# Performance work log

Measured on AMD Instinct MI355X. Metric: run time of the kernel, lower is better.

The kernel has to match this reference:

```python
import jax, jax.numpy as jnp
import numpy as np

N_NODES = 50000


def setup_inputs() -> dict:
    key = jax.random.key(0)
    k_x, k_e, k_w1, k_w2 = jax.random.split(key, 4)
    in_c, hid, out_c = 256, 128, 64
    x = jax.random.normal(k_x, (N_NODES, in_c), dtype=jnp.float32)
    edge_index = jax.random.randint(k_e, (2, 800000), 0, N_NODES, dtype=jnp.int64)
    # Glorot-ish scaled weights (faithful to GCNConv default init scale)
    W1 = jax.random.normal(k_w1, (in_c, hid), dtype=jnp.float32) * (1.0 / np.sqrt(in_c))
    b1 = jnp.zeros((hid,), dtype=jnp.float32)
    W2 = jax.random.normal(k_w2, (hid, out_c), dtype=jnp.float32) * (1.0 / np.sqrt(hid))
    b2 = jnp.zeros((out_c,), dtype=jnp.float32)
    return {"x": x, "edge_index": edge_index, "W1": W1, "b1": b1, "W2": W2, "b2": b2}


def _gcn_norm(edge_index, n_nodes):
    # Add self loops, compute symmetric normalization D^-1/2 A D^-1/2.
    loop = jnp.arange(n_nodes, dtype=edge_index.dtype)
    src = jnp.concatenate([edge_index[0], loop])
    dst = jnp.concatenate([edge_index[1], loop])
    deg = jax.ops.segment_sum(jnp.ones_like(dst, dtype=jnp.float32), dst,
                              num_segments=n_nodes)
    dis = jnp.where(deg > 0, jax.lax.rsqrt(deg), 0.0)  # deg_inv_sqrt
    norm = dis[src] * dis[dst]  # [E + N]
    return src, dst, norm


def _gcn_conv(x, W, b, src, dst, norm, n_nodes):
    h = x @ W                                  # [N, F_out] dense transform first
    msgs = h[src] * norm[:, None]              # edge-wise gather + scale
    agg = jax.ops.segment_sum(msgs, dst, num_segments=n_nodes)  # scatter-add
    return agg + b


def reference(x, edge_index, W1, b1, W2, b2):
    n = x.shape[0]
    src, dst, norm = _gcn_norm(edge_index, n)  # cached=True: same norm both layers
    h = _gcn_conv(x, W1, b1, src, dst, norm, n)
    h = jax.nn.relu(h)
    # Dropout is identity in eval mode (deterministic reference)
    return _gcn_conv(h, W2, b2, src, dst, norm, n)
```

## Files before the change

kernel.cpp:

```cpp
#include <hip/hip_runtime.h>


#define IN_C 256
#define HID 128
#define OUTC 64
#define NBLK 256

typedef __attribute__((ext_vector_type(8))) short short8;
typedef __attribute__((ext_vector_type(4))) float f32x4;

__device__ __forceinline__ void gload_lds16(const void* src, void* dst) {
    __builtin_amdgcn_global_load_lds(
        (const __attribute__((address_space(1))) unsigned int*)src,
        (__attribute__((address_space(3))) unsigned int*)dst, 16, 0, 0);
}

__device__ __forceinline__ void bf16split(float f, ushort& h, ushort& l) {
    unsigned u = __float_as_uint(f);
    h = (ushort)(u >> 16);
    float hf = __uint_as_float(u & 0xFFFF0000u);
    unsigned v = __float_as_uint(f - hf);
    l = (ushort)((v + 0x7FFF + ((v >> 16) & 1)) >> 16);
}

__device__ __forceinline__ void cvt8(float4 f0, float4 f1, short8& hi8, short8& lo8) {
    float ff[8];
    *(float4*)&ff[0] = f0; *(float4*)&ff[4] = f1;
    unsigned* hp = (unsigned*)&hi8;
    unsigned* lp = (unsigned*)&lo8;
    #pragma unroll
    for (int i = 0; i < 4; ++i) {
        unsigned u0 = __float_as_uint(ff[2 * i]), u1 = __float_as_uint(ff[2 * i + 1]);
        unsigned hf0 = u0 & 0xFFFF0000u, hf1 = u1 & 0xFFFF0000u;
        hp[i] = (u0 >> 16) | hf1;
        float r0 = ff[2 * i]     - __uint_as_float(hf0);
        float r1 = ff[2 * i + 1] - __uint_as_float(hf1);
        lp[i] = (__float_as_uint(r0) >> 16) | (__float_as_uint(r1) & 0xFFFF0000u);
    }
}

__device__ __forceinline__ ushort f2bf(float f) {
    unsigned u = __float_as_uint(f);
    return (ushort)((u + 0x7FFF + ((u >> 16) & 1)) >> 16);
}
__device__ __forceinline__ float bf2f(ushort u) {
    return __uint_as_float((unsigned)u << 16);
}

__device__ __forceinline__ int edge_at(const void* ei, long long idx, int is32) {
    return is32 ? ((const int*)ei)[idx] : (int)((const long long*)ei)[idx];
}

__device__ __forceinline__ int detect32(const void* ei) {
    const unsigned long long* p = (const unsigned long long*)ei;
    int is32 = 0;
    for (int i = 0; i < 64; ++i)
        if (p[i] >> 32) { is32 = 1; break; }
    return is32;
}

__global__ __launch_bounds__(256) void wtrans_kernel(const float* __restrict__ W1,
                                                     const float* __restrict__ W2,
                                                     ushort* __restrict__ wf1,
                                                     ushort* __restrict__ wf2,
                                                     ushort* __restrict__ h1sent,
                                                     ushort* __restrict__ h2sent) {
    int id = blockIdx.x * 256 + threadIdx.x;
    if (id < 8192) {
        int lane = id & 63, r = id >> 6;
        int pl = r & 1, nt = (r >> 1) & 7, kidx = r >> 4;
        int n = nt * 16 + (lane & 15);
        int kb = kidx * 32 + (lane >> 4) * 8;
        ushort v[8];
        #pragma unroll
        for (int j = 0; j < 8; ++j) {
            ushort h, l; bf16split(W1[(kb + j) * HID + n], h, l);
            v[j] = pl ? l : h;
        }
        *(short8*)&wf1[(size_t)id * 8] = *(short8*)v;
    } else if (id < 10240) {
        int id2 = id - 8192;
        int lane = id2 & 63, r = id2 >> 6;
        int pl = r & 1, nt = (r >> 1) & 3, kidx = r >> 3;
        int n = nt * 16 + (lane & 15);
        int kb = kidx * 32 + (lane >> 4) * 8;
        ushort v[8];
        #pragma unroll
        for (int j = 0; j < 8; ++j) {
            ushort h, l; bf16split(W2[(kb + j) * OUTC + n], h, l);
            v[j] = pl ? l : h;
        }
        *(short8*)&wf2[(size_t)id2 * 8] = *(short8*)v;
    } else if (id < 10368) {
        h1sent[id - 10240] = 0;
    } else if (id < 10432) {
        h2sent[id - 10368] = 0;
    }
}

__global__ __launch_bounds__(256) void bin_count(const void* ei,
                                                 int* __restrict__ blkcnt, int E, int nb) {
    __shared__ int h[256];
    __shared__ int s_is32;
    int t = threadIdx.x;
    h[t] = 0;
    if (t == 0) s_is32 = detect32(ei);
    __syncthreads();
    int is32 = s_is32;
    int chunk = (E + gridDim.x - 1) / gridDim.x;
    long long s0 = (long long)blockIdx.x * chunk;
    long long s1 = s0 + chunk; if (s1 > E) s1 = E;
    for (long long e = s0 + t; e < s1; e += 256) {
        int d = edge_at(ei, (long long)E + e, is32);
        atomicAdd(&h[d >> 8], 1);
    }
    __syncthreads();
    if (t < nb) blkcnt[t * NBLK + blockIdx.x] = h[t];
}

__global__ __launch_bounds__(256) void bin_scan(int* __restrict__ blkcnt,
                                                int* __restrict__ bbase, int nb) {
    __shared__ int sh[256];
    int t = threadIdx.x;
    int tot = 0;
    if (t < nb) {
        int4* p = (int4*)&blkcnt[t * NBLK];
        int run = 0;
        for (int i = 0; i < NBLK / 4; ++i) {
            int4 v = p[i]; int4 o;
            o.x = run; run += v.x; o.y = run; run += v.y;
            o.z = run; run += v.z; o.w = run; run += v.w;
            p[i] = o;
        }
        tot = run;
    }
    sh[t] = tot;
    __syncthreads();
    for (int d = 1; d < 256; d <<= 1) {
        int add = (t >= d) ? sh[t - d] : 0;
        __syncthreads();
        sh[t] += add;
        __syncthreads();
    }
    if (t < nb) {
        bbase[t] = sh[t] - tot;
        if (t == nb - 1) bbase[nb] = sh[t];
    }
}

__global__ __launch_bounds__(256) void bin_scatter(const void* ei,
                                                   const int* __restrict__ blkcnt,
                                                   const int* __restrict__ bbase,
                                                   unsigned* __restrict__ coarse, int E, int nb) {
    __shared__ int cur[256];
    __shared__ int s_is32;
    int t = threadIdx.x;
    if (t < nb) cur[t] = bbase[t] + blkcnt[t * NBLK + blockIdx.x];
    if (t == 0) s_is32 = detect32(ei);
    __syncthreads();
    int is32 = s_is32;
    int chunk = (E + gridDim.x - 1) / gridDim.x;
    long long s0 = (long long)blockIdx.x * chunk;
    long long s1 = s0 + chunk; if (s1 > E) s1 = E;
    for (long long e = s0 + t; e < s1; e += 256) {
        int s = edge_at(ei, e, is32);
        int d = edge_at(ei, (long long)E + e, is32);
        int p = atomicAdd(&cur[d >> 8], 1);
        coarse[p] = (unsigned)s | ((unsigned)(d & 255) << 17);
    }
}

__global__ __launch_bounds__(256) void fine_kernel(const unsigned* __restrict__ coarse,
                                                   const int* __restrict__ bbase,
                                                   int2* __restrict__ rp2,
                                                   float* __restrict__ dis,
                                                   int* __restrict__ epk, int N, int nb) {
    __shared__ int h[256], cur[256], sh[256];
    int b = blockIdx.x, t = threadIdx.x;
    int nb0 = b << 8;
    int e0b = bbase[b], e1b = bbase[b + 1];
    int obase0 = e0b + b * 4096;
    h[t] = 0;
    __syncthreads();
    for (int e = e0b + t; e < e1b; e += 256)
        atomicAdd(&h[(coarse[e] >> 17) & 0xFF], 1);
    __syncthreads();
    int cnt = h[t];
    int pad = (cnt + 15) & ~15;
    sh[t] = pad;
    __syncthreads();
    for (int d = 1; d < 256; d <<= 1) {
        int add = (t >= d) ? sh[t - d] : 0;
        __syncthreads();
        sh[t] += add;
        __syncthreads();
    }
    int base = obase0 + sh[t] - pad;
    int node = nb0 + t;
    if (node < N) {
        rp2[node] = make_int2(base, pad);
        dis[node] = rsqrtf((float)cnt + 1.0f);
    }
    cur[t] = base;
    __syncthreads();
    for (int e = e0b + t; e < e1b; e += 256) {
        unsigned r = coarse[e];
        int p = atomicAdd(&cur[(r >> 17) & 0xFF], 1);
        epk[p] = (int)(r & 0x1FFFF);
    }
    __syncthreads();
    for (int p = cur[t]; p < base + pad; ++p) epk[p] = N;
}

__global__ __launch_bounds__(256) void gemm1_mfma(const float* __restrict__ X,
                                                  const ushort* __restrict__ wf1,
                                                  const float* __restrict__ dis,
                                                  ushort* __restrict__ HB, int N) {
    __shared__ float xs[64 * 64];
    int t = threadIdx.x;
    int lane = t & 63, w = t >> 6;
    int m_off = (w >> 1) * 32, n_off = (w & 1) * 64;
    long long row0 = (long long)blockIdx.x * 64;
    f32x4 acc[2][4] = {};
    for (int k0i = 0; k0i < 4; ++k0i) {
        __syncthreads();
        #pragma unroll
        for (int i = 0; i < 4; ++i) {
            int lrow = w * 16 + i * 4 + (lane >> 4);
            long long gr = row0 + lrow; if (gr >= N) gr = N - 1;
            int gchunk = (lane & 15) ^ (lrow & 7);
            gload_lds16(X + gr * IN_C + k0i * 64 + gchunk * 4,
                        xs + (w * 16 + i * 4) * 64);
        }
        __syncthreads();
        #pragma unroll
        for (int kk = 0; kk < 2; ++kk) {
            int kidx = k0i * 2 + kk;
            short8 ah[2], al[2], bh[4], bl[4];
            #pragma unroll
            for (int ni = 0; ni < 4; ++ni) {
                int nt = (n_off >> 4) + ni;
                const ushort* bp = wf1 + (size_t)(kidx * 16 + nt * 2) * 512 + lane * 8;
                bh[ni] = *(const short8*)bp;
                bl[ni] = *(const short8*)(bp + 512);
            }
            #pragma unroll
            for (int mi = 0; mi < 2; ++mi) {
                int r = m_off + mi * 16 + (lane & 15);
                int s = r & 7;
                int c0 = kk * 8 + (lane >> 4) * 2;
                float4 f0 = *(float4*)((char*)xs + r * 256 + ((c0 ^ s) * 16));
                float4 f1 = *(float4*)((char*)xs + r * 256 + (((c0 + 1) ^ s) * 16));
                cvt8(f0, f1, ah[mi], al[mi]);
            }
            #pragma unroll
            for (int mi = 0; mi < 2; ++mi)
                #pragma unroll
                for (int ni = 0; ni < 4; ++ni) {
                    acc[mi][ni] = __builtin_amdgcn_mfma_f32_16x16x32_bf16(ah[mi], bh[ni], acc[mi][ni], 0, 0, 0);
                    acc[mi][ni] = __builtin_amdgcn_mfma_f32_16x16x32_bf16(ah[mi], bl[ni], acc[mi][ni], 0, 0, 0);
                    acc[mi][ni] = __builtin_amdgcn_mfma_f32_16x16x32_bf16(al[mi], bh[ni], acc[mi][ni], 0, 0, 0);
                }
        }
    }
    int cr = (lane >> 4) * 4, cc = lane & 15;
    #pragma unroll
    for (int mi = 0; mi < 2; ++mi)
        #pragma unroll
        for (int j = 0; j < 4; ++j) {
            long long gr = row0 + m_off + mi * 16 + cr + j;
            if (gr < N) {
                float dv = dis[gr];
                #pragma unroll
                for (int ni = 0; ni < 4; ++ni) {
                    int col = n_off + ni * 16 + cc;
                    HB[gr * HID + col] = f2bf(acc[mi][ni][j] * dv);
                }
            }
        }
}

__global__ __launch_bounds__(256) void gemm2_mfma(const ushort* __restrict__ Ah,
                                                  const ushort* __restrict__ Al,
                                                  const ushort* __restrict__ wf2,
                                                  const float* __restrict__ dis,
                                                  ushort* __restrict__ HB, int N) {
    __shared__ ushort ash[64 * 64], asl[64 * 64];
    int t = threadIdx.x;
    int lane = t & 63, w = t >> 6;
    int m_off = (w >> 1) * 32, n_off = (w & 1) * 32;
    long long row0 = (long long)blockIdx.x * 64;
    f32x4 acc[2][2] = {};
    for (int k0i = 0; k0i < 2; ++k0i) {
        __syncthreads();
        #pragma unroll
        for (int i = 0; i < 2; ++i) {
            int rbase = w * 16 + i * 8;
            long long gr = row0 + rbase + (lane >> 3);
            size_t so = (size_t)gr * 128 + k0i * 64 + (lane & 7) * 8;
            gload_lds16(Ah + so, ash + rbase * 64);
            gload_lds16(Al + so, asl + rbase * 64);
        }
        __syncthreads();
        #pragma unroll
        for (int kk = 0; kk < 2; ++kk) {
            int kidx = k0i * 2 + kk;
            short8 ah[2], al[2], bh[2], bl[2];
            #pragma unroll
            for (int ni = 0; ni < 2; ++ni) {
                int nt = (n_off >> 4) + ni;
                const ushort* bp = wf2 + (size_t)(kidx * 8 + nt * 2) * 512 + lane * 8;
                bh[ni] = *(const short8*)bp;
                bl[ni] = *(const short8*)(bp + 512);
            }
            #pragma unroll
            for (int mi = 0; mi < 2; ++mi) {
                int r = m_off + mi * 16 + (lane & 15);
                int pos = (kk * 4 + (lane >> 4)) ^ (r & 7);
                ah[mi] = *(short8*)((char*)ash + r * 128 + pos * 16);
                al[mi] = *(short8*)((char*)asl + r * 128 + pos * 16);
            }
            #pragma unroll
            for (int mi = 0; mi < 2; ++mi)
                #pragma unroll
                for (int ni = 0; ni < 2; ++ni) {
                    acc[mi][ni] = __builtin_amdgcn_mfma_f32_16x16x32_bf16(ah[mi], bh[ni], acc[mi][ni], 0, 0, 0);
                    acc[mi][ni] = __builtin_amdgcn_mfma_f32_16x16x32_bf16(ah[mi], bl[ni], acc[mi][ni], 0, 0, 0);
                    acc[mi][ni] = __builtin_amdgcn_mfma_f32_16x16x32_bf16(al[mi], bh[ni], acc[mi][ni], 0, 0, 0);
                }
        }
    }
    int cr = (lane >> 4) * 4, cc = lane & 15;
    #pragma unroll
    for (int mi = 0; mi < 2; ++mi)
        #pragma unroll
        for (int j = 0; j < 4; ++j) {
            long long gr = row0 + m_off + mi * 16 + cr + j;
            if (gr < N) {
                float dv = dis[gr];
                #pragma unroll
                for (int ni = 0; ni < 2; ++ni)
                    HB[gr * OUTC + n_off + ni * 16 + cc] = f2bf(acc[mi][ni][j] * dv);
            }
        }
}

__global__ __launch_bounds__(256) void seg_agg_l1(const ushort* __restrict__ H,
                                                  const float* __restrict__ dis,
                                                  const int2* __restrict__ rp2,
                                                  const int* __restrict__ epk,
                                                  const float* __restrict__ bias,
                                                  ushort* __restrict__ outH,
                                                  ushort* __restrict__ outL,
                                                  int N) {
    int lane = threadIdx.x & 63;
    int node = (int)(((long long)blockIdx.x * blockDim.x + threadIdx.x) >> 6);
    if (node >= N) return;
    const unsigned* hl = (const unsigned*)H + lane;
    unsigned v0 = hl[(size_t)node * 64];
    float a0 = bf2f((ushort)v0), a1 = bf2f((ushort)(v0 >> 16));
    int2 r2 = rp2[node];
    int e = r2.x, end = r2.x + r2.y;
    for (; e < end; e += 64) {
        int rem = end - e;
        int rec = epk[min(e + lane, end - 1)];
        int m = min(64, rem);
        for (int u0 = 0; u0 < m; u0 += 16) {
            unsigned hv[16];
            #pragma unroll
            for (int u = 0; u < 16; ++u) {
                int s = __builtin_amdgcn_readlane(rec, u0 + u);
                hv[u] = hl[(size_t)s * 64];
            }
            #pragma unroll
            for (int u = 0; u < 16; ++u) {
                a0 += bf2f((ushort)hv[u]);
                a1 += bf2f((ushort)(hv[u] >> 16));
            }
        }
    }
    float dn = dis[node];
    int c0 = lane * 2;
    float2 bb = *(const float2*)&bias[c0];
    float p0 = fmaxf(dn * a0 + bb.x, 0.f);
    float p1 = fmaxf(dn * a1 + bb.y, 0.f);
    unsigned u0b = __float_as_uint(p0), u1b = __float_as_uint(p1);
    unsigned h0 = u0b >> 16, h1 = u1b >> 16;
    float r0 = p0 - __uint_as_float(u0b & 0xFFFF0000u);
    float r1 = p1 - __uint_as_float(u1b & 0xFFFF0000u);
    unsigned l0 = __float_as_uint(r0) >> 16, l1 = __float_as_uint(r1) >> 16;
    int sl = c0 >> 6, el = c0 & 63;
    int ch = ((el >> 3) ^ (node & 7));
    size_t pos = (size_t)node * 128 + sl * 64 + ch * 8 + (el & 7);
    *(unsigned*)&outH[pos] = h0 | (h1 << 16);
    *(unsigned*)&outL[pos] = l0 | (l1 << 16);
}

__global__ __launch_bounds__(256) void seg_agg_l2(const ushort* __restrict__ H,
                                                  const float* __restrict__ dis,
                                                  const int2* __restrict__ rp2,
                                                  const int* __restrict__ epk,
                                                  const float* __restrict__ bias,
                                                  float* __restrict__ outF,
                                                  int N) {
    int lane = threadIdx.x & 63;
    int wv = (int)(((long long)blockIdx.x * blockDim.x + threadIdx.x) >> 6);
    int n0 = wv * 2;
    if (n0 >= N) return;
    int n1 = n0 + 1;
    int has1 = (n1 < N);
    int half = lane >> 5;
    int myn = half ? (has1 ? n1 : N) : n0;
    int f2 = (lane & 31) * 2;
    unsigned v0 = *(const unsigned*)&H[(size_t)myn * 64 + f2];
    float a0 = bf2f((ushort)v0), a1 = bf2f((ushort)(v0 >> 16));
    int2 rA = rp2[n0];
    int2 rB = has1 ? rp2[n1] : make_int2(0, 0);
    int eA = rA.x, endA = rA.x + rA.y;
    int eB = rB.x, endB = rB.x + rB.y;
    while (eA < endA || eB < endB) {
        int remA = endA - eA, remB = endB - eB;
        int mA = remA > 0 ? min(64, remA) : 0;
        int mB = remB > 0 ? min(64, remB) : 0;
        int recA = mA ? epk[min(eA + lane, endA - 1)] : 0;
        int recB = mB ? epk[min(eB + lane, endB - 1)] : 0;
        int m = max(mA, mB);
        for (int u0 = 0; u0 < m; u0 += 16) {
            unsigned hv[16];
            #pragma unroll
            for (int u = 0; u < 16; ++u) {
                int idx = u0 + u;
                int sA = (idx < mA) ? __builtin_amdgcn_readlane(recA, idx) : N;
                int sB = (idx < mB) ? __builtin_amdgcn_readlane(recB, idx) : N;
                int s = half ? sB : sA;
                hv[u] = *(const unsigned*)&H[(size_t)s * 64 + f2];
            }
            #pragma unroll
            for (int u = 0; u < 16; ++u) {
                a0 += bf2f((ushort)hv[u]);
                a1 += bf2f((ushort)(hv[u] >> 16));
            }
        }
        eA += mA; eB += mB;
    }
    if (!half || has1) {
        int sn = half ? n1 : n0;
        float dn = dis[sn];
        float2 bb = *(const float2*)&bias[f2];
        float2 o;
        o.x = dn * a0 + bb.x;
        o.y = dn * a1 + bb.y;
        *(float2*)&outF[(size_t)sn * 64 + f2] = o;
    }
}

extern "C" void kernel_launch(void* const* d_in, const int* in_sizes, int n_in,
                              void* d_out, int out_size, void* d_ws, size_t ws_size,
                              hipStream_t stream) {
    const float* x  = (const float*)d_in[0];
    const void*  ei = d_in[1];
    const float* W1 = (const float*)d_in[2];
    const float* b1 = (const float*)d_in[3];
    const float* W2 = (const float*)d_in[4];
    const float* b2 = (const float*)d_in[5];
    float* out = (float*)d_out;
    int N = in_sizes[0] / IN_C;
    int E = in_sizes[1] / 2;
    int nb = (N + 255) >> 8;
    int nblk64 = (N + 63) / 64;
    int N_pad = nblk64 * 64;

    char* ws = (char*)d_ws;
    size_t off = 0;
    auto alloc = [&](size_t bytes) {
        void* p = ws + off;
        off += ((bytes + 255) / 256) * 256;
        return p;
    };
    int*      blkcnt  = (int*)alloc((size_t)nb * NBLK * 4);
    int*      bbase   = (int*)alloc(((size_t)nb + 1) * 4);
    int2*     rp2     = (int2*)alloc((size_t)N * 8);
    float*    dis     = (float*)alloc((size_t)N * 4);
    unsigned* coarse  = (unsigned*)alloc((size_t)E * 4);
    int*      epk     = (int*)alloc(((size_t)E + (size_t)nb * 4096) * 4);
    ushort*   wf1     = (ushort*)alloc(131072);
    ushort*   wf2     = (ushort*)alloc(32768);
    ushort*   H1b     = (ushort*)alloc(((size_t)N + 1) * HID * 2);
    ushort*   Ah      = (ushort*)alloc((size_t)N_pad * 128 * 2);
    ushort*   Al      = (ushort*)alloc((size_t)N_pad * 128 * 2);
    ushort*   H2b     = (ushort*)alloc(((size_t)N + 1) * OUTC * 2);

    wtrans_kernel<<<41, 256, 0, stream>>>(W1, W2, wf1, wf2,
                                          H1b + (size_t)N * HID,
                                          H2b + (size_t)N * OUTC);
    bin_count<<<NBLK, 256, 0, stream>>>(ei, blkcnt, E, nb);
    bin_scan<<<1, 256, 0, stream>>>(blkcnt, bbase, nb);
    bin_scatter<<<NBLK, 256, 0, stream>>>(ei, blkcnt, bbase, coarse, E, nb);
    fine_kernel<<<nb, 256, 0, stream>>>(coarse, bbase, rp2, dis, epk, N, nb);
    gemm1_mfma<<<nblk64, 256, 0, stream>>>(x, wf1, dis, H1b, N);

    int agg1_blocks = (int)(((long long)N * 64 + 255) / 256);
    seg_agg_l1<<<agg1_blocks, 256, 0, stream>>>(H1b, dis, rp2, epk, b1, Ah, Al, N);
    gemm2_mfma<<<nblk64, 256, 0, stream>>>(Ah, Al, wf2, dis, H2b, N);
    int waves2 = (N + 1) / 2;
    int agg2_blocks = (int)(((long long)waves2 * 64 + 255) / 256);
    seg_agg_l2<<<agg2_blocks, 256, 0, stream>>>(H2b, dis, rp2, epk, b2, out, N);
}
```

Measured before the change: 139.0 us.

## Fuse CSR build kernels into one cooperative kernel with grid syncs

Merges the weight-transform, bin count, bin scan, bin scatter and fine-sort kernels into a single cooperative launch of 256 blocks, separated by grid.sync barriers. This removes four kernel launches and the gaps between them in the preprocessing chain. In exchange, the scan runs on a single block while every other block waits at a grid barrier. The fine stage also needs nb (196) ≤ 256 blocks, and the whole grid must be co-resident for the cooperative launch to work.

Result: slower. 235.2 us (+69.3%).

```diff
diff --git a/kernel.cpp b/kernel.cpp
--- a/kernel.cpp
+++ b/kernel.cpp
@@ -1,4 +1,7 @@
 #include <hip/hip_runtime.h>
+#include <hip/hip_cooperative_groups.h>
+
+namespace cg = cooperative_groups;
 
 
 #define IN_C 256
@@ -59,157 +62,151 @@
     return is32;
 }
 
-__global__ __launch_bounds__(256) void wtrans_kernel(const float* __restrict__ W1,
-                                                     const float* __restrict__ W2,
-                                                     ushort* __restrict__ wf1,
-                                                     ushort* __restrict__ wf2,
-                                                     ushort* __restrict__ h1sent,
-                                                     ushort* __restrict__ h2sent) {
-    int id = blockIdx.x * 256 + threadIdx.x;
-    if (id < 8192) {
-        int lane = id & 63, r = id >> 6;
-        int pl = r & 1, nt = (r >> 1) & 7, kidx = r >> 4;
-        int n = nt * 16 + (lane & 15);
-        int kb = kidx * 32 + (lane >> 4) * 8;
-        ushort v[8];
-        #pragma unroll
-        for (int j = 0; j < 8; ++j) {
-            ushort h, l; bf16split(W1[(kb + j) * HID + n], h, l);
-            v[j] = pl ? l : h;
-        }
-        *(short8*)&wf1[(size_t)id * 8] = *(short8*)v;
-    } else if (id < 10240) {
-        int id2 = id - 8192;
-        int lane = id2 & 63, r = id2 >> 6;
-        int pl = r & 1, nt = (r >> 1) & 3, kidx = r >> 3;
-        int n = nt * 16 + (lane & 15);
-        int kb = kidx * 32 + (lane >> 4) * 8;
-        ushort v[8];
-        #pragma unroll
-        for (int j = 0; j < 8; ++j) {
-            ushort h, l; bf16split(W2[(kb + j) * OUTC + n], h, l);
-            v[j] = pl ? l : h;
-        }
-        *(short8*)&wf2[(size_t)id2 * 8] = *(short8*)v;
-    } else if (id < 10368) {
-        h1sent[id - 10240] = 0;
-    } else if (id < 10432) {
-        h2sent[id - 10368] = 0;
-    }
-}
-
-__global__ __launch_bounds__(256) void bin_count(const void* ei,
-                                                 int* __restrict__ blkcnt, int E, int nb) {
-    __shared__ int h[256];
+__global__ __launch_bounds__(256) void csr_coop(const void* ei,
+                                                const float* __restrict__ W1,
+                                                const float* __restrict__ W2,
+                                                ushort* __restrict__ wf1,
+                                                ushort* __restrict__ wf2,
+                                                ushort* __restrict__ h1sent,
+                                                ushort* __restrict__ h2sent,
+                                                int* __restrict__ blkcnt,
+                                                int* __restrict__ bbase,
+                                                int2* __restrict__ rp2,
+                                                float* __restrict__ dis,
+                                                unsigned* __restrict__ coarse,
+                                                int* __restrict__ epk,
+                                                int E, int N, int nb) {
+    cg::grid_group grid = cg::this_grid();
+    __shared__ int sh_a[256], sh_b[256], sh_c[256];
     __shared__ int s_is32;
-    int t = threadIdx.x;
-    h[t] = 0;
-    if (t == 0) s_is32 = detect32(ei);
-    __syncthreads();
-    int is32 = s_is32;
-    int chunk = (E + gridDim.x - 1) / gridDim.x;
-    long long s0 = (long long)blockIdx.x * chunk;
+    int b = blockIdx.x, t = threadIdx.x;
+    int chunk = (E + NBLK - 1) / NBLK;
+    long long s0 = (long long)b * chunk;
     long long s1 = s0 + chunk; if (s1 > E) s1 = E;
-    for (long long e = s0 + t; e < s1; e += 256) {
-        int d = edge_at(ei, (long long)E + e, is32);
-        atomicAdd(&h[d >> 8], 1);
-    }
-    __syncthreads();
-    if (t < nb) blkcnt[t * NBLK + blockIdx.x] = h[t];
-}
-
-__global__ __launch_bounds__(256) void bin_scan(int* __restrict__ blkcnt,
-                                                int* __restrict__ bbase, int nb) {
-    __shared__ int sh[256];
-    int t = threadIdx.x;
-    int tot = 0;
-    if (t < nb) {
-        int4* p = (int4*)&blkcnt[t * NBLK];
-        int run = 0;
-        for (int i = 0; i < NBLK / 4; ++i) {
-            int4 v = p[i]; int4 o;
-            o.x = run; run += v.x; o.y = run; run += v.y;
-            o.z = run; run += v.z; o.w = run; run += v.w;
-            p[i] = o;
-        }
-        tot = run;
-    }
-    sh[t] = tot;
-    __syncthreads();
-    for (int d = 1; d < 256; d <<= 1) {
-        int add = (t >= d) ? sh[t - d] : 0;
-        __syncthreads();
-        sh[t] += add;
-        __syncthreads();
-    }
-    if (t < nb) {
-        bbase[t] = sh[t] - tot;
-        if (t == nb - 1) bbase[nb] = sh[t];
-    }
-}
-
-__global__ __launch_bounds__(256) void bin_scatter(const void* ei,
-                                                   const int* __restrict__ blkcnt,
-                                                   const int* __restrict__ bbase,
-                                                   unsigned* __restrict__ coarse, int E, int nb) {
-    __shared__ int cur[256];
-    __shared__ int s_is32;
-    int t = threadIdx.x;
-    if (t < nb) cur[t] = bbase[t] + blkcnt[t * NBLK + blockIdx.x];
-    if (t == 0) s_is32 = detect32(ei);
-    __syncthreads();
-    int is32 = s_is32;
-    int chunk = (E + gridDim.x - 1) / gridDim.x;
-    long long s0 = (long long)blockIdx.x * chunk;
-    long long s1 = s0 + chunk; if (s1 > E) s1 = E;
-    for (long long e = s0 + t; e < s1; e += 256) {
-        int s = edge_at(ei, e, is32);
-        int d = edge_at(ei, (long long)E + e, is32);
-        int p = atomicAdd(&cur[d >> 8], 1);
-        coarse[p] = (unsigned)s | ((unsigned)(d & 255) << 17);
-    }
-}
-
-__global__ __launch_bounds__(256) void fine_kernel(const unsigned* __restrict__ coarse,
-                                                   const int* __restrict__ bbase,
-                                                   int2* __restrict__ rp2,
-                                                   float* __restrict__ dis,
-                                                   int* __restrict__ epk, int N, int nb) {
-    __shared__ int h[256], cur[256], sh[256];
-    int b = blockIdx.x, t = threadIdx.x;
-    int nb0 = b << 8;
-    int e0b = bbase[b], e1b = bbase[b + 1];
-    int obase0 = e0b + b * 4096;
-    h[t] = 0;
-    __syncthreads();
-    for (int e = e0b + t; e < e1b; e += 256)
-        atomicAdd(&h[(coarse[e] >> 17) & 0xFF], 1);
-    __syncthreads();
-    int cnt = h[t];
-    int pad = (cnt + 15) & ~15;
-    sh[t] = pad;
-    __syncthreads();
-    for (int d = 1; d < 256; d <<= 1) {
-        int add = (t >= d) ? sh[t - d] : 0;
-        __syncthreads();
-        sh[t] += add;
-        __syncthreads();
-    }
-    int base = obase0 + sh[t] - pad;
-    int node = nb0 + t;
-    if (node < N) {
-        rp2[node] = make_int2(base, pad);
-        dis[node] = rsqrtf((float)cnt + 1.0f);
-    }
-    cur[t] = base;
-    __syncthreads();
-    for (int e = e0b + t; e < e1b; e += 256) {
-        unsigned r = coarse[e];
-        int p = atomicAdd(&cur[(r >> 17) & 0xFF], 1);
-        epk[p] = (int)(r & 0x1FFFF);
-    }
-    __syncthreads();
-    for (int p = cur[t]; p < base + pad; ++p) epk[p] = N;
+
+    {
+        int id = t * 256 + b;
+        if (id < 8192) {
+            int lane = id & 63, r = id >> 6;
+            int pl = r & 1, nt = (r >> 1) & 7, kidx = r >> 4;
+            int n = nt * 16 + (lane & 15);
+            int kb = kidx * 32 + (lane >> 4) * 8;
+            ushort v[8];
+            #pragma unroll
+            for (int j = 0; j < 8; ++j) {
+                ushort h, l; bf16split(W1[(kb + j) * HID + n], h, l);
+                v[j] = pl ? l : h;
+            }
+            *(short8*)&wf1[(size_t)id * 8] = *(short8*)v;
+        } else if (id < 10240) {
+            int id2 = id - 8192;
+            int lane = id2 & 63, r = id2 >> 6;
+            int pl = r & 1, nt = (r >> 1) & 3, kidx = r >> 3;
+            int n = nt * 16 + (lane & 15);
+            int kb = kidx * 32 + (lane >> 4) * 8;
+            ushort v[8];
+            #pragma unroll
+            for (int j = 0; j < 8; ++j) {
+                ushort h, l; bf16split(W2[(kb + j) * OUTC + n], h, l);
+                v[j] = pl ? l : h;
+            }
+            *(short8*)&wf2[(size_t)id2 * 8] = *(short8*)v;
+        } else if (id < 10368) {
+            h1sent[id - 10240] = 0;
+        } else if (id < 10432) {
+            h2sent[id - 10368] = 0;
+        }
+    }
+    {
+        sh_a[t] = 0;
+        if (t == 0) s_is32 = detect32(ei);
+        __syncthreads();
+        int is32 = s_is32;
+        for (long long e = s0 + t; e < s1; e += 256) {
+            int d = edge_at(ei, (long long)E + e, is32);
+            atomicAdd(&sh_a[d >> 8], 1);
+        }
+        __syncthreads();
+        if (t < nb) blkcnt[t * NBLK + b] = sh_a[t];
+    }
+    grid.sync();
+
+    if (b == 0) {
+        int tot = 0;
+        if (t < nb) {
+            int4* p = (int4*)&blkcnt[t * NBLK];
+            int run = 0;
+            for (int i = 0; i < NBLK / 4; ++i) {
+                int4 v = p[i]; int4 o;
+                o.x = run; run += v.x; o.y = run; run += v.y;
+                o.z = run; run += v.z; o.w = run; run += v.w;
+                p[i] = o;
+            }
+            tot = run;
+        }
+        sh_b[t] = tot;
+        __syncthreads();
+        for (int d = 1; d < 256; d <<= 1) {
+            int add = (t >= d) ? sh_b[t - d] : 0;
+            __syncthreads();
+            sh_b[t] += add;
+            __syncthreads();
+        }
+        if (t < nb) {
+            bbase[t] = sh_b[t] - tot;
+            if (t == nb - 1) bbase[nb] = sh_b[t];
+        }
+    }
+    grid.sync();
+
+    {
+        if (t < nb) sh_a[t] = bbase[t] + blkcnt[t * NBLK + b];
+        __syncthreads();
+        int is32 = s_is32;
+        for (long long e = s0 + t; e < s1; e += 256) {
+            int s = edge_at(ei, e, is32);
+            int d = edge_at(ei, (long long)E + e, is32);
+            int p = atomicAdd(&sh_a[d >> 8], 1);
+            coarse[p] = (unsigned)s | ((unsigned)(d & 255) << 17);
+        }
+    }
+    grid.sync();
+
+    if (b < nb) {
+        int nb0 = b << 8;
+        int e0b = bbase[b], e1b = bbase[b + 1];
+        int obase0 = e0b + b * 4096;
+        sh_a[t] = 0;
+        __syncthreads();
+        for (int e = e0b + t; e < e1b; e += 256)
+            atomicAdd(&sh_a[(coarse[e] >> 17) & 0xFF], 1);
+        __syncthreads();
+        int cnt = sh_a[t];
+        int pad = (cnt + 15) & ~15;
+        sh_b[t] = pad;
+        __syncthreads();
+        for (int d = 1; d < 256; d <<= 1) {
+            int add = (t >= d) ? sh_b[t - d] : 0;
+            __syncthreads();
+            sh_b[t] += add;
+            __syncthreads();
+        }
+        int base = obase0 + sh_b[t] - pad;
+        int node = nb0 + t;
+        if (node < N) {
+            rp2[node] = make_int2(base, pad);
+            dis[node] = rsqrtf((float)cnt + 1.0f);
+        }
+        sh_c[t] = base;
+        __syncthreads();
+        for (int e = e0b + t; e < e1b; e += 256) {
+            unsigned r = coarse[e];
+            int p = atomicAdd(&sh_c[(r >> 17) & 0xFF], 1);
+            epk[p] = (int)(r & 0x1FFFF);
+        }
+        __syncthreads();
+        for (int p = sh_c[t]; p < base + pad; ++p) epk[p] = N;
+    }
 }
 
 __global__ __launch_bounds__(256) void gemm1_mfma(const float* __restrict__ X,
@@ -457,8 +454,8 @@
 extern "C" void kernel_launch(void* const* d_in, const int* in_sizes, int n_in,
                               void* d_out, int out_size, void* d_ws, size_t ws_size,
                               hipStream_t stream) {
+    const void*  ei = d_in[1];
     const float* x  = (const float*)d_in[0];
-    const void*  ei = d_in[1];
     const float* W1 = (const float*)d_in[2];
     const float* b1 = (const float*)d_in[3];
     const float* W2 = (const float*)d_in[4];
@@ -490,15 +487,16 @@
     ushort*   Al      = (ushort*)alloc((size_t)N_pad * 128 * 2);
     ushort*   H2b     = (ushort*)alloc(((size_t)N + 1) * OUTC * 2);
 
-    wtrans_kernel<<<41, 256, 0, stream>>>(W1, W2, wf1, wf2,
-                                          H1b + (size_t)N * HID,
-                                          H2b + (size_t)N * OUTC);
-    bin_count<<<NBLK, 256, 0, stream>>>(ei, blkcnt, E, nb);
-    bin_scan<<<1, 256, 0, stream>>>(blkcnt, bbase, nb);
-    bin_scatter<<<NBLK, 256, 0, stream>>>(ei, blkcnt, bbase, coarse, E, nb);
-    fine_kernel<<<nb, 256, 0, stream>>>(coarse, bbase, rp2, dis, epk, N, nb);
+    ushort* h1sent = H1b + (size_t)N * HID;
+    ushort* h2sent = H2b + (size_t)N * OUTC;
+    void* args[] = { (void*)&ei, (void*)&W1, (void*)&W2, (void*)&wf1, (void*)&wf2,
+                     (void*)&h1sent, (void*)&h2sent, (void*)&blkcnt, (void*)&bbase,
+                     (void*)&rp2, (void*)&dis, (void*)&coarse, (void*)&epk,
+                     (void*)&E, (void*)&N, (void*)&nb };
+    hipLaunchCooperativeKernel((const void*)csr_coop, dim3(NBLK), dim3(256),
+                               args, 0, stream);
+
     gemm1_mfma<<<nblk64, 256, 0, stream>>>(x, wf1, dis, H1b, N);
-
     int agg1_blocks = (int)(((long long)N * 64 + 255) / 256);
     seg_agg_l1<<<agg1_blocks, 256, 0, stream>>>(H1b, dis, rp2, epk, b1, Ah, Al, N);
     gemm2_mfma<<<nblk64, 256, 0, stream>>>(Ah, Al, wf2, dis, H2b, N);
```
